# Performance work log

Measured on AMD Instinct MI355X. Metric: run time of the kernel, lower is better.

## Reference

```python
import jax, jax.numpy as jnp
import numpy as np

H = 256   # hidden_size
B = 64    # batch_size
LP = 2048 # passage length
LQ = 64   # question length


def _linear(x, W, b):
    # torch nn.Linear: y = x @ W.T + b
    return jnp.matmul(x, W.T) + b


def _gru_cell(x, h, w_ih, w_hh, b_ih, b_hh):
    # torch GRUCell semantics: x is input, h is hidden state
    gi = jnp.matmul(x, w_ih.T) + b_ih   # [B, 3*2H]
    gh = jnp.matmul(h, w_hh.T) + b_hh
    i_r, i_z, i_n = jnp.split(gi, 3, axis=-1)
    h_r, h_z, h_n = jnp.split(gh, 3, axis=-1)
    r = jax.nn.sigmoid(i_r + h_r)
    z = jax.nn.sigmoid(i_z + h_z)
    n = jnp.tanh(i_n + r * h_n)
    return (1.0 - z) * n + z * h


def setup_inputs() -> dict:
    key = jax.random.key(0)
    ks = jax.random.split(key, 17)
    s = lambda i, shape: jax.random.normal(ks[i], shape, dtype=jnp.float32) * 0.05
    return {
        "passEnc": jax.random.normal(ks[0], (LP, B, 2 * H), dtype=jnp.float32),
        "quesEnc": jax.random.normal(ks[1], (LQ, B, 2 * H), dtype=jnp.float32),
        "WQu_W": s(2, (H, 2 * H)), "WQu_b": s(3, (H,)),
        "WQv_W": s(4, (H, H)),     "WQv_b": s(5, (H,)),
        "WPh_W": s(6, (H, 2 * H)), "WPh_b": s(7, (H,)),
        "Wah_W": s(8, (H, 2 * H)), "Wah_b": s(9, (H,)),
        "Vt1": s(10, (B, H, 1)),
        "Vt2": s(11, (B, H, 1)),
        "VQr": s(12, (1, 1, H)),
        "gru_wih": s(13, (6 * H, 2 * H)), "gru_whh": s(14, (6 * H, 2 * H)),
        "gru_bih": s(15, (6 * H,)),       "gru_bhh": s(16, (6 * H,)),
    }


def reference(passEnc, quesEnc, WQu_W, WQu_b, WQv_W, WQv_b, WPh_W, WPh_b,
              Wah_W, Wah_b, Vt1, Vt2, VQr, gru_wih, gru_whh, gru_bih, gru_bhh):
    # --- question-aware initial state rQ ---
    # temp: [lQ, B, H] (VQr path broadcasts over lQ and B)
    temp = jnp.tanh(_linear(quesEnc, WQu_W, WQu_b) + _linear(VQr, WQv_W, WQv_b))
    sQ = jnp.einsum('qbh,bh->bq', temp, Vt1[..., 0])          # [B, lQ]
    a = jax.nn.softmax(sQ, axis=1)
    rQ = jnp.einsum('bq,qbd->bd', a, quesEnc)                 # [B, 2H]

    passP = _linear(passEnc, WPh_W, WPh_b)                    # [lP, B, H], reused both steps

    def pointer_step(rQ):
        temp2 = jnp.tanh(passP + _linear(rQ, Wah_W, Wah_b))   # [lP, B, H]
        sP = jnp.einsum('pbh,bh->bp', temp2, Vt2[..., 0])     # [B, lP]
        aP = jax.nn.softmax(sP, axis=1)
        ct = jnp.einsum('bp,pbd->bd', aP, passEnc)            # [B, 2H]
        return aP, ct

    aP1, ct = pointer_step(rQ)
    rQ = _gru_cell(rQ, ct, gru_wih, gru_whh, gru_bih, gru_bhh)
    aP2, _ = pointer_step(rQ)
    return (aP1, aP2)


if __name__ == "__main__":
    out = reference(**setup_inputs())
    print(out[0].shape, out[1].shape)
```

## Files before the change

kernel.cpp:

```cpp
#include <hip/hip_runtime.h>
#include <math.h>


constexpr int Bn   = 64;
constexpr int Hn   = 256;
constexpr int D2H  = 512;
constexpr int LPn  = 2048;
constexpr int LQn  = 64;

typedef __attribute__((ext_vector_type(8))) short bf16x8;
typedef __attribute__((ext_vector_type(4))) float f32x4;

__device__ inline float waveAllSum(float v) {
  #pragma unroll
  for (int o = 32; o > 0; o >>= 1) v += __shfl_xor(v, o, 64);
  return v;
}
__device__ inline float waveAllMax(float v) {
  #pragma unroll
  for (int o = 32; o > 0; o >>= 1) v = fmaxf(v, __shfl_xor(v, o, 64));
  return v;
}

__device__ inline short f2bf_rtne(float f) {
  union { float f; unsigned u; } v; v.f = f;
  unsigned r = v.u + 0x7FFF + ((v.u >> 16) & 1);
  return (short)(r >> 16);
}

__device__ inline unsigned pk2(float lo, float hi) {
  union { float f; unsigned u; } a, b; a.f = lo; b.f = hi;
  return __builtin_amdgcn_perm(b.u + 0x8000u, a.u + 0x8000u, 0x07060302u);
}
__device__ inline bf16x8 cvt8(f32x4 a0, f32x4 a1) {
  union { unsigned u[4]; bf16x8 v; } r;
  r.u[0] = pk2(a0[0], a0[1]);
  r.u[1] = pk2(a0[2], a0[3]);
  r.u[2] = pk2(a1[0], a1[1]);
  r.u[3] = pk2(a1[2], a1[3]);
  return r.v;
}

__global__ __launch_bounds__(256) void k_wcvt(const float* __restrict__ WQu,
                                              const float* __restrict__ WPh,
                                              short* __restrict__ q2,
                                              short* __restrict__ p2) {
  int s = blockIdx.x * 256 + threadIdx.x;
  const float* W; short* D; int slot;
  if (s < 16384) { W = WQu; D = q2; slot = s; }
  else           { W = WPh; D = p2; slot = s - 16384; }
  int l    = slot & 63;
  int rest = slot >> 6;
  int h    = rest & 1;
  int k0i  = (rest >> 1) & 7;
  int wj   = rest >> 4;
  int l15  = l & 15, quad = l >> 4;
  int n = (wj >> 2) * 64 + (wj & 3) * 16 + l15;
  int k = k0i * 64 + h * 32 + quad * 8;
  f32x4 f0 = *(const f32x4*)&W[n * 512 + k];
  f32x4 f1 = *(const f32x4*)&W[n * 512 + k + 4];
  bf16x8 o;
  o[0] = f2bf_rtne(f0[0]); o[1] = f2bf_rtne(f0[1]);
  o[2] = f2bf_rtne(f0[2]); o[3] = f2bf_rtne(f0[3]);
  o[4] = f2bf_rtne(f1[0]); o[5] = f2bf_rtne(f1[1]);
  o[6] = f2bf_rtne(f1[2]); o[7] = f2bf_rtne(f1[3]);
  *(bf16x8*)&D[slot * 8] = o;
}

__global__ __launch_bounds__(256) void k_v2(const float* __restrict__ VQr,
                                            const float* __restrict__ WQv_W,
                                            const float* __restrict__ WQv_b,
                                            float* __restrict__ v2) {
  __shared__ float s[256];
  int t = threadIdx.x;
  s[t] = VQr[t];
  __syncthreads();
  float acc = WQv_b[t];
  for (int k = 0; k < 256; ++k) acc += s[k] * WQv_W[t * 256 + k];
  v2[t] = acc;
}

__global__ __launch_bounds__(256, 3) void k_mfma_fused(
    const float* __restrict__ A,
    const short* __restrict__ Wb2,
    const float* __restrict__ bias,
    const float* __restrict__ u,
    const float* __restrict__ vt,
    float* __restrict__ C,
    float* __restrict__ sOut,
    int ustride, int sstride)
{
  __shared__ float sred[4][64];
  const int tid  = threadIdx.x;
  const int w    = tid >> 6;
  const int l    = tid & 63;
  const int l15  = l & 15;
  const int quad = l >> 4;
  const long bm  = (long)blockIdx.x * 64;

  f32x4 acc[4][4];
  #pragma unroll
  for (int i = 0; i < 4; ++i)
    #pragma unroll
    for (int j = 0; j < 4; ++j)
      acc[i][j] = (f32x4)0.f;

  const float* arow[4];
  #pragma unroll
  for (int i = 0; i < 4; ++i)
    arow[i] = A + (size_t)(bm + i * 16 + l15) * 512 + quad * 8;
  const short* bptr = Wb2 + (size_t)w * 4 * 8192 + l * 8;

  for (int k0i = 0; k0i < 8; ++k0i) {
    const int k0 = k0i * 64;
    f32x4 a0[4][2], a1[4][2];
    #pragma unroll
    for (int i = 0; i < 4; ++i)
      #pragma unroll
      for (int h = 0; h < 2; ++h) {
        const float* p = arow[i] + k0 + h * 32;
        a0[i][h] = *(const f32x4*)p;
        a1[i][h] = *(const f32x4*)(p + 4);
      }
    bf16x8 bfr[2][4];
    #pragma unroll
    for (int h = 0; h < 2; ++h)
      #pragma unroll
      for (int j = 0; j < 4; ++j)
        bfr[h][j] = *(const bf16x8*)(bptr + j * 8192 + k0i * 1024 + h * 512);
    #pragma unroll
    for (int h = 0; h < 2; ++h) {
      bf16x8 af[4];
      #pragma unroll
      for (int i = 0; i < 4; ++i) af[i] = cvt8(a0[i][h], a1[i][h]);
      #pragma unroll
      for (int i = 0; i < 4; ++i)
        #pragma unroll
        for (int j = 0; j < 4; ++j)
          acc[i][j] = __builtin_amdgcn_mfma_f32_16x16x32_bf16(af[i], bfr[h][j], acc[i][j], 0, 0, 0);
    }
  }

  float srow[4][4];
  #pragma unroll
  for (int i = 0; i < 4; ++i) {
    #pragma unroll
    for (int r = 0; r < 4; ++r) {
      const int row = i * 16 + quad * 4 + r;
      float s_acc = 0.f;
      #pragma unroll
      for (int j = 0; j < 4; ++j) {
        const int n = w * 64 + j * 16 + l15;
        float val = acc[i][j][r] + bias[n];
        if (C) C[(bm + row) * 256 + n] = val;
        s_acc += tanhf(val + u[ustride * row + n]) * vt[row * 256 + n];
      }
      srow[i][r] = s_acc;
    }
  }
  #pragma unroll
  for (int off = 1; off < 16; off <<= 1)
    #pragma unroll
    for (int i = 0; i < 4; ++i)
      #pragma unroll
      for (int r = 0; r < 4; ++r)
        srow[i][r] += __shfl_xor(srow[i][r], off, 64);
  if (l15 == 0)
    #pragma unroll
    for (int i = 0; i < 4; ++i)
      #pragma unroll
      for (int r = 0; r < 4; ++r)
        sred[w][i * 16 + quad * 4 + r] = srow[i][r];
  __syncthreads();
  if (tid < 64)
    sOut[(size_t)tid * sstride + blockIdx.x] =
        sred[0][tid] + sred[1][tid] + sred[2][tid] + sred[3][tid];
}

__global__ __launch_bounds__(256) void k_rq_u1(const float* __restrict__ sQ,
                                               const float* __restrict__ quesEnc,
                                               const float* __restrict__ Wah,
                                               const float* __restrict__ Wah_b,
                                               float* __restrict__ rQ,
                                               float* __restrict__ u1) {
  int b = blockIdx.x, tid = threadIdx.x;
  __shared__ float s_a[LQn];
  __shared__ float s_r[D2H];
  if (tid < 64) {
    float s = sQ[b * LQn + tid];
    float m = waveAllMax(s);
    float e = expf(s - m);
    float sum = waveAllSum(e);
    s_a[tid] = e / sum;
  }
  __syncthreads();
  #pragma unroll
  for (int rep = 0; rep < 2; ++rep) {
    int d = tid + rep * 256;
    float acc = 0.f;
    for (int q = 0; q < LQn; ++q)
      acc += s_a[q] * quesEnc[(size_t)(q * Bn + b) * D2H + d];
    s_r[d] = acc;
    rQ[b * D2H + d] = acc;
  }
  __syncthreads();
  float accu = Wah_b[tid];
  const float* wr = Wah + (size_t)tid * 512;
  for (int k4 = 0; k4 < 128; ++k4) {
    f32x4 wv = *(const f32x4*)&wr[k4 * 4];
    f32x4 rv = *(const f32x4*)&s_r[k4 * 4];
    accu += wv[0] * rv[0] + wv[1] * rv[1] + wv[2] * rv[2] + wv[3] * rv[3];
  }
  u1[b * Hn + tid] = accu;
}

__global__ __launch_bounds__(256) void k_sp(const float* __restrict__ passP,
                                            const float* __restrict__ u,
                                            const float* __restrict__ Vt2,
                                            float* __restrict__ sP) {
  int flat = blockIdx.x * 4 + (threadIdx.x >> 6);
  int lane = threadIdx.x & 63;
  int b = flat & (Bn - 1);
  int p = flat >> 6;
  float4 v  = *(const float4*)&passP[(size_t)flat * Hn + lane * 4];
  float4 uu = *(const float4*)&u[b * Hn + lane * 4];
  float4 vt = *(const float4*)&Vt2[b * Hn + lane * 4];
  float s = tanhf(v.x + uu.x) * vt.x + tanhf(v.y + uu.y) * vt.y +
            tanhf(v.z + uu.z) * vt.z + tanhf(v.w + uu.w) * vt.w;
  s = waveAllSum(s);
  if (lane == 0) sP[b * LPn + p] = s;
}

__global__ __launch_bounds__(256) void k_softmax(const float* __restrict__ sP,
                                                 float* __restrict__ out) {
  int b = blockIdx.x, tid = threadIdx.x;
  int lane = tid & 63, wid = tid >> 6;
  __shared__ float red[4];
  float v[8];
  float m = -1e30f;
  #pragma unroll
  for (int i = 0; i < 8; ++i) {
    v[i] = sP[b * LPn + i * 256 + tid];
    m = fmaxf(m, v[i]);
  }
  m = waveAllMax(m);
  if (lane == 0) red[wid] = m;
  __syncthreads();
  m = fmaxf(fmaxf(red[0], red[1]), fmaxf(red[2], red[3]));
  float s = 0.f;
  #pragma unroll
  for (int i = 0; i < 8; ++i) { v[i] = expf(v[i] - m); s += v[i]; }
  s = waveAllSum(s);
  __syncthreads();
  if (lane == 0) red[wid] = s;
  __syncthreads();
  s = red[0] + red[1] + red[2] + red[3];
  float inv = 1.0f / s;
  #pragma unroll
  for (int i = 0; i < 8; ++i) out[b * LPn + i * 256 + tid] = v[i] * inv;
}

__global__ __launch_bounds__(256) void k_ct(const float* __restrict__ aP,
                                            const float* __restrict__ passEnc,
                                            float* __restrict__ ct) {
  int b = blockIdx.x, pc = blockIdx.y, tid = threadIdx.x;
  int dg = tid & 127;
  int pg = tid >> 7;
  f32x4 acc = (f32x4)0.f;
  for (int pp = 0; pp < 64; ++pp) {
    int p = pc * 128 + pg * 64 + pp;
    float a = aP[b * LPn + p];
    acc += a * *(const f32x4*)&passEnc[((size_t)p * Bn + b) * D2H + dg * 4];
  }
  __shared__ f32x4 sacc[256];
  sacc[tid] = acc;
  __syncthreads();
  if (pg == 0) {
    acc += sacc[tid + 128];
    float* dst = &ct[b * D2H + dg * 4];
    atomicAdd(dst + 0, acc[0]);
    atomicAdd(dst + 1, acc[1]);
    atomicAdd(dst + 2, acc[2]);
    atomicAdd(dst + 3, acc[3]);
  }
}

__global__ __launch_bounds__(256) void k_gru(const float* __restrict__ rQ,
                                             const float* __restrict__ ct,
                                             const float* __restrict__ wih,
                                             const float* __restrict__ whh,
                                             const float* __restrict__ bih,
                                             const float* __restrict__ bhh,
                                             float* __restrict__ rQ2) {
  int m = blockIdx.x;
  int j = blockIdx.y * 256 + threadIdx.x;
  __shared__ float sx[D2H], sh[D2H];
  sx[threadIdx.x]       = rQ[m * D2H + threadIdx.x];
  sx[threadIdx.x + 256] = rQ[m * D2H + threadIdx.x + 256];
  sh[threadIdx.x]       = ct[m * D2H + threadIdx.x];
  sh[threadIdx.x + 256] = ct[m * D2H + threadIdx.x + 256];
  __syncthreads();
  float gr = bih[j], gz = bih[512 + j], gn = bih[1024 + j];
  float hr = bhh[j], hz = bhh[512 + j], hn = bhh[1024 + j];
  const float* wr0 = wih + (size_t)j * 512;
  const float* wr1 = wih + (size_t)(512 + j) * 512;
  const float* wr2 = wih + (size_t)(1024 + j) * 512;
  const float* vr0 = whh + (size_t)j * 512;
  const float* vr1 = whh + (size_t)(512 + j) * 512;
  const float* vr2 = whh + (size_t)(1024 + j) * 512;
  for (int k4 = 0; k4 < 128; ++k4) {
    f32x4 x = *(const f32x4*)&sx[k4 * 4];
    f32x4 h = *(const f32x4*)&sh[k4 * 4];
    f32x4 w0 = *(const f32x4*)&wr0[k4 * 4];
    f32x4 w1 = *(const f32x4*)&wr1[k4 * 4];
    f32x4 w2 = *(const f32x4*)&wr2[k4 * 4];
    f32x4 v0 = *(const f32x4*)&vr0[k4 * 4];
    f32x4 v1 = *(const f32x4*)&vr1[k4 * 4];
    f32x4 v2 = *(const f32x4*)&vr2[k4 * 4];
    #pragma unroll
    for (int e = 0; e < 4; ++e) {
      gr += w0[e] * x[e]; gz += w1[e] * x[e]; gn += w2[e] * x[e];
      hr += v0[e] * h[e]; hz += v1[e] * h[e]; hn += v2[e] * h[e];
    }
  }
  float r = 1.f / (1.f + expf(-(gr + hr)));
  float z = 1.f / (1.f + expf(-(gz + hz)));
  float nn = tanhf(gn + r * hn);
  rQ2[m * D2H + j] = (1.f - z) * nn + z * sh[j];
}

__global__ __launch_bounds__(256) void k_u2(const float* __restrict__ rQ2,
                                            const float* __restrict__ Wah,
                                            const float* __restrict__ Wah_b,
                                            float* __restrict__ u2) {
  int m = blockIdx.x, n = threadIdx.x;
  __shared__ float s_r[D2H];
  s_r[n]       = rQ2[m * D2H + n];
  s_r[n + 256] = rQ2[m * D2H + n + 256];
  __syncthreads();
  float acc = Wah_b[n];
  const float* wr = Wah + (size_t)n * 512;
  for (int k4 = 0; k4 < 128; ++k4) {
    f32x4 wv = *(const f32x4*)&wr[k4 * 4];
    f32x4 rv = *(const f32x4*)&s_r[k4 * 4];
    acc += wv[0] * rv[0] + wv[1] * rv[1] + wv[2] * rv[2] + wv[3] * rv[3];
  }
  u2[m * Hn + n] = acc;
}

extern "C" void kernel_launch(void* const* d_in, const int* in_sizes, int n_in,
                              void* d_out, int out_size, void* d_ws, size_t ws_size,
                              hipStream_t stream) {
  const float* passEnc  = (const float*)d_in[0];
  const float* quesEnc  = (const float*)d_in[1];
  const float* WQu_W    = (const float*)d_in[2];
  const float* WQu_b    = (const float*)d_in[3];
  const float* WQv_W    = (const float*)d_in[4];
  const float* WQv_b    = (const float*)d_in[5];
  const float* WPh_W    = (const float*)d_in[6];
  const float* WPh_b    = (const float*)d_in[7];
  const float* Wah_W    = (const float*)d_in[8];
  const float* Wah_b    = (const float*)d_in[9];
  const float* Vt1      = (const float*)d_in[10];
  const float* Vt2      = (const float*)d_in[11];
  const float* VQr      = (const float*)d_in[12];
  const float* gru_wih  = (const float*)d_in[13];
  const float* gru_whh  = (const float*)d_in[14];
  const float* gru_bih  = (const float*)d_in[15];
  const float* gru_bhh  = (const float*)d_in[16];
  float* out = (float*)d_out;

  float* ws = (float*)d_ws;
  float* passP = ws;
  float* v2    = ws + 33554432;
  float* rQ    = v2 + 256;
  float* u1    = rQ + 32768;
  float* u2    = u1 + 16384;
  float* sP    = u2 + 16384;
  float* ct    = sP + 131072;
  float* rQ2   = ct + 32768;
  float* sQ    = rQ2 + 32768;
  short* wqu2  = (short*)(sQ + 4096);
  short* wph2  = wqu2 + 131072;

  k_wcvt<<<128, 256, 0, stream>>>(WQu_W, WPh_W, wqu2, wph2);
  k_v2<<<1, 256, 0, stream>>>(VQr, WQv_W, WQv_b, v2);

  k_mfma_fused<<<LQn, 256, 0, stream>>>(quesEnc, wqu2, WQu_b, v2, Vt1,
                                        nullptr, sQ, 0, LQn);
  k_rq_u1<<<Bn, 256, 0, stream>>>(sQ, quesEnc, Wah_W, Wah_b, rQ, u1);

  k_mfma_fused<<<LPn, 256, 0, stream>>>(passEnc, wph2, WPh_b, u1, Vt2,
                                        passP, sP, Hn, LPn);
  k_softmax<<<Bn, 256, 0, stream>>>(sP, out);

  hipMemsetAsync(ct, 0, Bn * D2H * sizeof(float), stream);
  k_ct<<<dim3(Bn, 16), 256, 0, stream>>>(out, passEnc, ct);

  k_gru<<<dim3(Bn, 2), 256, 0, stream>>>(rQ, ct, gru_wih, gru_whh,
                                         gru_bih, gru_bhh, rQ2);
  k_u2<<<Bn, 256, 0, stream>>>(rQ2, Wah_W, Wah_b, u2);

  k_sp<<<LPn * Bn / 4, 256, 0, stream>>>(passP, u2, Vt2, sP);
  k_softmax<<<Bn, 256, 0, stream>>>(sP, out + Bn * LPn);
}
```

Before: 924.0 us.

## Recompute passage projection instead of storing passP; add register double-buffering

The passage projection passP (128MB fp32) is no longer written out. The second pointer step reruns the fused MFMA GEMM on passEnc with u2, which replaces the k_sp kernel that read passP back. This trades about 256MB of write plus read traffic for a second bf16 GEMM that rereads passEnc (256MB). The MFMA main loop also prefetches the next K slice of A and B into registers, with occupancy lowered from 3 to 2 to fit them, and the k_ct loop gets an unroll pragma.

```diff
diff --git a/kernel.cpp b/kernel.cpp
--- a/kernel.cpp
+++ b/kernel.cpp
@@ -80,13 +80,12 @@
   v2[t] = acc;
 }
 
-__global__ __launch_bounds__(256, 3) void k_mfma_fused(
+__global__ __launch_bounds__(256, 2) void k_mfma_fused(
     const float* __restrict__ A,
     const short* __restrict__ Wb2,
     const float* __restrict__ bias,
     const float* __restrict__ u,
     const float* __restrict__ vt,
-    float* __restrict__ C,
     float* __restrict__ sOut,
     int ustride, int sstride)
 {
@@ -111,33 +110,65 @@
     arow[i] = A + (size_t)(bm + i * 16 + l15) * 512 + quad * 8;
   const short* bptr = Wb2 + (size_t)w * 4 * 8192 + l * 8;
 
+  f32x4  a_cur[4][2][2], a_nxt[4][2][2];
+  bf16x8 b_cur[2][4],    b_nxt[2][4];
+
+  #pragma unroll
+  for (int i = 0; i < 4; ++i)
+    #pragma unroll
+    for (int h = 0; h < 2; ++h) {
+      const float* p = arow[i] + h * 32;
+      a_cur[i][h][0] = *(const f32x4*)p;
+      a_cur[i][h][1] = *(const f32x4*)(p + 4);
+    }
+  #pragma unroll
+  for (int h = 0; h < 2; ++h)
+    #pragma unroll
+    for (int j = 0; j < 4; ++j)
+      b_cur[h][j] = *(const bf16x8*)(bptr + j * 8192 + h * 512);
+
+  #pragma unroll
   for (int k0i = 0; k0i < 8; ++k0i) {
-    const int k0 = k0i * 64;
-    f32x4 a0[4][2], a1[4][2];
-    #pragma unroll
-    for (int i = 0; i < 4; ++i)
-      #pragma unroll
-      for (int h = 0; h < 2; ++h) {
-        const float* p = arow[i] + k0 + h * 32;
-        a0[i][h] = *(const f32x4*)p;
-        a1[i][h] = *(const f32x4*)(p + 4);
-      }
-    bf16x8 bfr[2][4];
-    #pragma unroll
-    for (int h = 0; h < 2; ++h)
-      #pragma unroll
-      for (int j = 0; j < 4; ++j)
-        bfr[h][j] = *(const bf16x8*)(bptr + j * 8192 + k0i * 1024 + h * 512);
+    if (k0i < 7) {
+      const int k1 = (k0i + 1) * 64;
+      #pragma unroll
+      for (int i = 0; i < 4; ++i)
+        #pragma unroll
+        for (int h = 0; h < 2; ++h) {
+          const float* p = arow[i] + k1 + h * 32;
+          a_nxt[i][h][0] = *(const f32x4*)p;
+          a_nxt[i][h][1] = *(const f32x4*)(p + 4);
+        }
+      #pragma unroll
+      for (int h = 0; h < 2; ++h)
+        #pragma unroll
+        for (int j = 0; j < 4; ++j)
+          b_nxt[h][j] = *(const bf16x8*)(bptr + j * 8192 + (k0i + 1) * 1024 + h * 512);
+    }
     #pragma unroll
     for (int h = 0; h < 2; ++h) {
       bf16x8 af[4];
       #pragma unroll
-      for (int i = 0; i < 4; ++i) af[i] = cvt8(a0[i][h], a1[i][h]);
+      for (int i = 0; i < 4; ++i) af[i] = cvt8(a_cur[i][h][0], a_cur[i][h][1]);
       #pragma unroll
       for (int i = 0; i < 4; ++i)
         #pragma unroll
         for (int j = 0; j < 4; ++j)
-          acc[i][j] = __builtin_amdgcn_mfma_f32_16x16x32_bf16(af[i], bfr[h][j], acc[i][j], 0, 0, 0);
+          acc[i][j] = __builtin_amdgcn_mfma_f32_16x16x32_bf16(af[i], b_cur[h][j], acc[i][j], 0, 0, 0);
+    }
+    if (k0i < 7) {
+      #pragma unroll
+      for (int i = 0; i < 4; ++i)
+        #pragma unroll
+        for (int h = 0; h < 2; ++h) {
+          a_cur[i][h][0] = a_nxt[i][h][0];
+          a_cur[i][h][1] = a_nxt[i][h][1];
+        }
+      #pragma unroll
+      for (int h = 0; h < 2; ++h)
+        #pragma unroll
+        for (int j = 0; j < 4; ++j)
+          b_cur[h][j] = b_nxt[h][j];
     }
   }
 
@@ -152,7 +183,6 @@
       for (int j = 0; j < 4; ++j) {
         const int n = w * 64 + j * 16 + l15;
         float val = acc[i][j][r] + bias[n];
-        if (C) C[(bm + row) * 256 + n] = val;
         s_acc += tanhf(val + u[ustride * row + n]) * vt[row * 256 + n];
       }
       srow[i][r] = s_acc;
@@ -214,23 +244,6 @@
   u1[b * Hn + tid] = accu;
 }
 
-__global__ __launch_bounds__(256) void k_sp(const float* __restrict__ passP,
-                                            const float* __restrict__ u,
-                                            const float* __restrict__ Vt2,
-                                            float* __restrict__ sP) {
-  int flat = blockIdx.x * 4 + (threadIdx.x >> 6);
-  int lane = threadIdx.x & 63;
-  int b = flat & (Bn - 1);
-  int p = flat >> 6;
-  float4 v  = *(const float4*)&passP[(size_t)flat * Hn + lane * 4];
-  float4 uu = *(const float4*)&u[b * Hn + lane * 4];
-  float4 vt = *(const float4*)&Vt2[b * Hn + lane * 4];
-  float s = tanhf(v.x + uu.x) * vt.x + tanhf(v.y + uu.y) * vt.y +
-            tanhf(v.z + uu.z) * vt.z + tanhf(v.w + uu.w) * vt.w;
-  s = waveAllSum(s);
-  if (lane == 0) sP[b * LPn + p] = s;
-}
-
 __global__ __launch_bounds__(256) void k_softmax(const float* __restrict__ sP,
                                                  float* __restrict__ out) {
   int b = blockIdx.x, tid = threadIdx.x;
@@ -267,6 +280,7 @@
   int dg = tid & 127;
   int pg = tid >> 7;
   f32x4 acc = (f32x4)0.f;
+  #pragma unroll 8
   for (int pp = 0; pp < 64; ++pp) {
     int p = pc * 128 + pg * 64 + pp;
     float a = aP[b * LPn + p];
@@ -371,8 +385,7 @@
   float* out = (float*)d_out;
 
   float* ws = (float*)d_ws;
-  float* passP = ws;
-  float* v2    = ws + 33554432;
+  float* v2    = ws;
   float* rQ    = v2 + 256;
   float* u1    = rQ + 32768;
   float* u2    = u1 + 16384;
@@ -387,11 +400,11 @@
   k_v2<<<1, 256, 0, stream>>>(VQr, WQv_W, WQv_b, v2);
 
   k_mfma_fused<<<LQn, 256, 0, stream>>>(quesEnc, wqu2, WQu_b, v2, Vt1,
-                                        nullptr, sQ, 0, LQn);
+                                        sQ, 0, LQn);
   k_rq_u1<<<Bn, 256, 0, stream>>>(sQ, quesEnc, Wah_W, Wah_b, rQ, u1);
 
   k_mfma_fused<<<LPn, 256, 0, stream>>>(passEnc, wph2, WPh_b, u1, Vt2,
-                                        passP, sP, Hn, LPn);
+                                        sP, Hn, LPn);
   k_softmax<<<Bn, 256, 0, stream>>>(sP, out);
 
   hipMemsetAsync(ct, 0, Bn * D2H * sizeof(float), stream);
@@ -401,6 +414,7 @@
                                          gru_bih, gru_bhh, rQ2);
   k_u2<<<Bn, 256, 0, stream>>>(rQ2, Wah_W, Wah_b, u2);
 
-  k_sp<<<LPn * Bn / 4, 256, 0, stream>>>(passP, u2, Vt2, sP);
+  k_mfma_fused<<<LPn, 256, 0, stream>>>(passEnc, wph2, WPh_b, u2, Vt2,
+                                        sP, Hn, LPn);
   k_softmax<<<Bn, 256, 0, stream>>>(sP, out + Bn * LPn);
 }
```

Result: slower. 1.024 ms (+10.8%).
